# Kernel optimization log

Hardware: AMD Instinct MI355X
Metric: run time of the kernel (lower is better)

## Reference

```python
import jax, jax.numpy as jnp
import numpy as np

S = 2        # number of scales (init default)
ALPHA = 1.0  # loss weight (init default)


def _local_pod_ss(D, n_scales):
    """Sum of squares of (P_n - P_o) over all scales/windows.

    D = h_n - h_o, shape [B, C, W, H]. Because POD is linear in x,
    POD(h_n window) - POD(h_o window) == POD(D window), and the final
    torch.norm(P_n - P_o, 2) is the Frobenius norm over the full concat,
    so we accumulate squared window-POD values of D and sqrt at the end.
    Window sums are computed once via prefix sums (integral along one axis)
    instead of the original O(W^2 H^2) re-summation loop.
    """
    B, C, W, H = D.shape
    ss = jnp.zeros((), D.dtype)
    d = 1
    for s in range(n_scales):
        w, h = W // d, H // d
        if w == 0 or h == 0:
            break
        nI, nJ = W - w, H - h  # number of window start positions (torch range(0, W-w))
        if nI > 0 and nJ > 0:
            # 'left' term: sum over rows (dim=2) of each window, divided by w
            cs2 = jnp.pad(jnp.cumsum(D, axis=2), ((0, 0), (0, 0), (1, 0), (0, 0)))
            row = cs2[:, :, w:w + nI, :] - cs2[:, :, :nI, :]              # [B,C,nI,H]
            jidx = jnp.arange(nJ)[:, None] + jnp.arange(h)[None, :]       # [nJ,h]
            left = row[:, :, :, jidx] / w                                 # [B,C,nI,nJ,h]
            ss = ss + jnp.sum(left * left)
            # 'right' term: sum over cols (dim=3) of each window, divided by h
            cs3 = jnp.pad(jnp.cumsum(D, axis=3), ((0, 0), (0, 0), (0, 0), (1, 0)))
            col = cs3[:, :, :, h:h + nJ] - cs3[:, :, :, :nJ]              # [B,C,W,nJ]
            iidx = jnp.arange(nI)[:, None] + jnp.arange(w)[None, :]       # [nI,w]
            right = col[:, :, iidx, :] / h                                # [B,C,nI,w,nJ]
            ss = ss + jnp.sum(right * right)
        d *= 2
    return ss


def setup_inputs() -> dict:
    key = jax.random.key(0)
    k1, k2 = jax.random.split(key)
    new_f = jax.random.normal(k1, (16, 512, 32, 32), dtype=jnp.float32)
    old_f = jax.random.normal(k2, (16, 512, 32, 32), dtype=jnp.float32)
    return {"new_f": new_f, "old_f": old_f}


def reference(new_f, old_f):
    # forward loops over dict keys; here new_f/old_f model a single-key dict,
    # so loss = 1e-6 + local_pod(h_n, h_o) and divisor is len(new_f)+1 == 2.
    D = new_f - old_f
    loss = jnp.asarray(1e-6, new_f.dtype) + jnp.sqrt(_local_pod_ss(D, S))
    return ALPHA * loss / 2.0
```

## Files before the change

### kernel.cpp

```cpp
#include <hip/hip_runtime.h>
#include <math.h>


#define TILES_PER_BLOCK 8
#define TILE_STRIDE (32 * 33)

__global__ __launch_bounds__(256) void pod_partial(const float* __restrict__ nf,
                                                   const float* __restrict__ of,
                                                   float* __restrict__ partial) {
    __shared__ float ds[TILES_PER_BLOCK * TILE_STRIDE];
    const int tid = threadIdx.x;
    const size_t base = (size_t)blockIdx.x * (TILES_PER_BLOCK * 1024);

    const float4* nf4 = reinterpret_cast<const float4*>(nf + base);
    const float4* of4 = reinterpret_cast<const float4*>(of + base);
#pragma unroll
    for (int it = 0; it < (TILES_PER_BLOCK * 1024) / (256 * 4); ++it) {
        int e4 = it * 256 + tid;
        float4 a = nf4[e4];
        float4 b = of4[e4];
        int e = e4 * 4;
        int tile = e >> 10;
        int r = (e >> 5) & 31;
        int c = e & 31;
        float* dst = &ds[tile * TILE_STRIDE + r * 33 + c];
        dst[0] = a.x - b.x;
        dst[1] = a.y - b.y;
        dst[2] = a.z - b.z;
        dst[3] = a.w - b.w;
    }
    __syncthreads();

    float acc = 0.0f;

    {
        int tile = tid >> 5, col = tid & 31;
        const float* colp = &ds[tile * TILE_STRIDE + col];
        float v[32];
#pragma unroll
        for (int r = 0; r < 32; ++r) v[r] = colp[r * 33];
        float W = 0.0f;
#pragma unroll
        for (int r = 0; r < 16; ++r) W += v[r];
        float s2 = W * W;
#pragma unroll
        for (int i = 1; i < 16; ++i) { W += v[i + 15] - v[i - 1]; s2 += W * W; }
        float wl = (col < 16) ? (float)(col + 1) : (float)(31 - col);
        acc += wl * s2;
    }

    {
        int tile = tid >> 5, row = tid & 31;
        const float* rowp = &ds[tile * TILE_STRIDE + row * 33];
        float v[32];
#pragma unroll
        for (int c = 0; c < 32; ++c) v[c] = rowp[c];
        float W = 0.0f;
#pragma unroll
        for (int c = 0; c < 16; ++c) W += v[c];
        float s2 = W * W;
#pragma unroll
        for (int j = 1; j < 16; ++j) { W += v[j + 15] - v[j - 1]; s2 += W * W; }
        float wr = (row < 16) ? (float)(row + 1) : (float)(31 - row);
        acc += wr * s2;
    }

    acc *= (1.0f / 256.0f);

#pragma unroll
    for (int off = 32; off > 0; off >>= 1) acc += __shfl_down(acc, off, 64);
    __shared__ float wsum[4];
    if ((tid & 63) == 0) wsum[tid >> 6] = acc;
    __syncthreads();
    if (tid == 0) partial[blockIdx.x] = (wsum[0] + wsum[1]) + (wsum[2] + wsum[3]);
}

__global__ __launch_bounds__(256) void pod_final(const float* __restrict__ partial, int n,
                                                 float* __restrict__ out) {
    __shared__ float sh[256];
    int tid = threadIdx.x;
    float a = 0.0f;
    for (int i = tid; i < n; i += 256) a += partial[i];
    sh[tid] = a;
    __syncthreads();
    for (int s = 128; s > 0; s >>= 1) {
        if (tid < s) sh[tid] += sh[tid + s];
        __syncthreads();
    }
    if (tid == 0) out[0] = 0.5f * (1e-6f + sqrtf(sh[0]));
}

extern "C" void kernel_launch(void* const* d_in, const int* in_sizes, int n_in,
                              void* d_out, int out_size, void* d_ws, size_t ws_size,
                              hipStream_t stream) {
    const float* nf = (const float*)d_in[0];
    const float* of = (const float*)d_in[1];
    float* out = (float*)d_out;
    float* partial = (float*)d_ws;

    const int ntiles = 16 * 512;
    const int nblocks = ntiles / TILES_PER_BLOCK;

    hipLaunchKernelGGL(pod_partial, dim3(nblocks), dim3(256), 0, stream, nf, of, partial);
    hipLaunchKernelGGL(pod_final, dim3(1), dim3(256), 0, stream, partial, nblocks, out);
}
```

Baseline: 18.55 us.

## Fuse final reduction via last-block atomic counter and double-buffer tile chunks

Replaces the two-kernel partial and final reduction with one kernel in which the last block to finish, found through an atomic counter, sums the per-block partials. Each block now handles its 8 tiles as two chunks in separate shared-memory buffers, with the second chunk's global loads issued before the first chunk's compute so they overlap. Column and row work is now split across threads (half do columns, half rows) rather than each thread doing both. This adds a hipMemsetAsync on every call and a threadfence/atomic on every block. Block count is now derived from in_sizes, and the counter sits at the start of the workspace.

```diff
diff --git a/kernel.cpp b/kernel.cpp
--- a/kernel.cpp
+++ b/kernel.cpp
@@ -2,69 +2,88 @@
 #include <math.h>
 
 
-#define TILES_PER_BLOCK 8
-#define TILE_STRIDE (32 * 33)
+#define TILE_PAD 33
+#define TILE_STRIDE (32 * TILE_PAD)
+#define CHUNK_TILES 4
+#define TPB_TILES 8
+#define BLOCK_FLOATS (TPB_TILES * 1024)
 
-__global__ __launch_bounds__(256) void pod_partial(const float* __restrict__ nf,
-                                                   const float* __restrict__ of,
-                                                   float* __restrict__ partial) {
-    __shared__ float ds[TILES_PER_BLOCK * TILE_STRIDE];
+__device__ __forceinline__ float chunk_term(const float* __restrict__ buf, int tid) {
+    const int item = tid & 127;
+    const int tile = item >> 5;
+    const int lane = item & 31;
+    float v[32];
+    if (tid < 128) {
+        const float* p = &buf[tile * TILE_STRIDE + lane];
+#pragma unroll
+        for (int k = 0; k < 32; ++k) v[k] = p[k * TILE_PAD];
+    } else {
+        const float* p = &buf[tile * TILE_STRIDE + lane * TILE_PAD];
+#pragma unroll
+        for (int k = 0; k < 32; ++k) v[k] = p[k];
+    }
+    float W = 0.0f;
+#pragma unroll
+    for (int k = 0; k < 16; ++k) W += v[k];
+    float s2 = W * W;
+#pragma unroll
+    for (int i = 1; i < 16; ++i) { W += v[i + 15] - v[i - 1]; s2 += W * W; }
+    float wgt = (lane < 16) ? (float)(lane + 1) : (float)(31 - lane);
+    return wgt * s2;
+}
+
+__global__ __launch_bounds__(256) void pod_fused(const float* __restrict__ nf,
+                                                 const float* __restrict__ of,
+                                                 unsigned* __restrict__ counter,
+                                                 float* __restrict__ partial,
+                                                 float* __restrict__ out) {
+    __shared__ float ds[2][CHUNK_TILES * TILE_STRIDE];
     const int tid = threadIdx.x;
-    const size_t base = (size_t)blockIdx.x * (TILES_PER_BLOCK * 1024);
-
+    const size_t base = (size_t)blockIdx.x * BLOCK_FLOATS;
     const float4* nf4 = reinterpret_cast<const float4*>(nf + base);
     const float4* of4 = reinterpret_cast<const float4*>(of + base);
+
+    float4 a0[4], b0[4];
 #pragma unroll
-    for (int it = 0; it < (TILES_PER_BLOCK * 1024) / (256 * 4); ++it) {
+    for (int it = 0; it < 4; ++it) {
         int e4 = it * 256 + tid;
-        float4 a = nf4[e4];
-        float4 b = of4[e4];
-        int e = e4 * 4;
-        int tile = e >> 10;
-        int r = (e >> 5) & 31;
-        int c = e & 31;
-        float* dst = &ds[tile * TILE_STRIDE + r * 33 + c];
-        dst[0] = a.x - b.x;
-        dst[1] = a.y - b.y;
-        dst[2] = a.z - b.z;
-        dst[3] = a.w - b.w;
+        a0[it] = nf4[e4];
+        b0[it] = of4[e4];
+    }
+#pragma unroll
+    for (int it = 0; it < 4; ++it) {
+        int e = (it * 256 + tid) * 4;
+        int tile = e >> 10, r = (e >> 5) & 31, c = e & 31;
+        float* dst = &ds[0][tile * TILE_STRIDE + r * TILE_PAD + c];
+        dst[0] = a0[it].x - b0[it].x;
+        dst[1] = a0[it].y - b0[it].y;
+        dst[2] = a0[it].z - b0[it].z;
+        dst[3] = a0[it].w - b0[it].w;
+    }
+    float4 a1[4], b1[4];
+#pragma unroll
+    for (int it = 0; it < 4; ++it) {
+        int e4 = 1024 + it * 256 + tid;
+        a1[it] = nf4[e4];
+        b1[it] = of4[e4];
     }
     __syncthreads();
 
-    float acc = 0.0f;
+    float acc = chunk_term(&ds[0][0], tid);
 
-    {
-        int tile = tid >> 5, col = tid & 31;
-        const float* colp = &ds[tile * TILE_STRIDE + col];
-        float v[32];
 #pragma unroll
-        for (int r = 0; r < 32; ++r) v[r] = colp[r * 33];
-        float W = 0.0f;
-#pragma unroll
-        for (int r = 0; r < 16; ++r) W += v[r];
-        float s2 = W * W;
-#pragma unroll
-        for (int i = 1; i < 16; ++i) { W += v[i + 15] - v[i - 1]; s2 += W * W; }
-        float wl = (col < 16) ? (float)(col + 1) : (float)(31 - col);
-        acc += wl * s2;
+    for (int it = 0; it < 4; ++it) {
+        int e = (it * 256 + tid) * 4;
+        int tile = e >> 10, r = (e >> 5) & 31, c = e & 31;
+        float* dst = &ds[1][tile * TILE_STRIDE + r * TILE_PAD + c];
+        dst[0] = a1[it].x - b1[it].x;
+        dst[1] = a1[it].y - b1[it].y;
+        dst[2] = a1[it].z - b1[it].z;
+        dst[3] = a1[it].w - b1[it].w;
     }
+    __syncthreads();
 
-    {
-        int tile = tid >> 5, row = tid & 31;
-        const float* rowp = &ds[tile * TILE_STRIDE + row * 33];
-        float v[32];
-#pragma unroll
-        for (int c = 0; c < 32; ++c) v[c] = rowp[c];
-        float W = 0.0f;
-#pragma unroll
-        for (int c = 0; c < 16; ++c) W += v[c];
-        float s2 = W * W;
-#pragma unroll
-        for (int j = 1; j < 16; ++j) { W += v[j + 15] - v[j - 1]; s2 += W * W; }
-        float wr = (row < 16) ? (float)(row + 1) : (float)(31 - row);
-        acc += wr * s2;
-    }
-
+    acc += chunk_term(&ds[1][0], tid);
     acc *= (1.0f / 256.0f);
 
 #pragma unroll
@@ -72,22 +91,31 @@
     __shared__ float wsum[4];
     if ((tid & 63) == 0) wsum[tid >> 6] = acc;
     __syncthreads();
-    if (tid == 0) partial[blockIdx.x] = (wsum[0] + wsum[1]) + (wsum[2] + wsum[3]);
-}
 
-__global__ __launch_bounds__(256) void pod_final(const float* __restrict__ partial, int n,
-                                                 float* __restrict__ out) {
-    __shared__ float sh[256];
-    int tid = threadIdx.x;
-    float a = 0.0f;
-    for (int i = tid; i < n; i += 256) a += partial[i];
-    sh[tid] = a;
+    __shared__ unsigned last;
+    if (tid == 0) {
+        float total = (wsum[0] + wsum[1]) + (wsum[2] + wsum[3]);
+        partial[blockIdx.x] = total;
+        __threadfence();
+        unsigned old = atomicAdd(counter, 1u);
+        last = (old == gridDim.x - 1) ? 1u : 0u;
+    }
     __syncthreads();
-    for (int s = 128; s > 0; s >>= 1) {
-        if (tid < s) sh[tid] += sh[tid + s];
+
+    if (last) {
+        __threadfence();
+        float s = 0.0f;
+        for (unsigned i = tid; i < gridDim.x; i += 256)
+            s += partial[i];
+        __shared__ float sh[256];
+        sh[tid] = s;
         __syncthreads();
+        for (int st = 128; st > 0; st >>= 1) {
+            if (tid < st) sh[tid] += sh[tid + st];
+            __syncthreads();
+        }
+        if (tid == 0) out[0] = 0.5f * (1e-6f + sqrtf(sh[0]));
     }
-    if (tid == 0) out[0] = 0.5f * (1e-6f + sqrtf(sh[0]));
 }
 
 extern "C" void kernel_launch(void* const* d_in, const int* in_sizes, int n_in,
@@ -96,11 +124,13 @@
     const float* nf = (const float*)d_in[0];
     const float* of = (const float*)d_in[1];
     float* out = (float*)d_out;
-    float* partial = (float*)d_ws;
 
-    const int ntiles = 16 * 512;
-    const int nblocks = ntiles / TILES_PER_BLOCK;
+    unsigned* counter = (unsigned*)d_ws;
+    float* partial = (float*)d_ws + 64;
 
-    hipLaunchKernelGGL(pod_partial, dim3(nblocks), dim3(256), 0, stream, nf, of, partial);
-    hipLaunchKernelGGL(pod_final, dim3(1), dim3(256), 0, stream, partial, nblocks, out);
+    const int nblocks = in_sizes[0] / BLOCK_FLOATS;
+
+    hipMemsetAsync(counter, 0, sizeof(unsigned), stream);
+    hipLaunchKernelGGL(pod_fused, dim3(nblocks), dim3(256), 0, stream,
+                       nf, of, counter, partial, out);
 }
```

Result: slower. 53.04 us (+185.9%).

## Fuse final reduction into main kernel via fixed-point atomics and last-block finish

Applied to the files above, without the earlier changes.

Replaces the two-kernel partial-sum plus single-block final reduction with one kernel. Each block adds its partial into a 64-bit fixed-point atomic accumulator, and a completion counter lets the last block compute the sqrt output. All global loads are now issued up front into registers before the shared-memory stores, giving more memory-level parallelism. This removes a kernel launch and the serial tail reduction, but adds a memset, atomic contention, and quantization error from the fixed-point scaling; the ordering between the two atomics relies on an asm dependency trick rather than a fence.

```diff
diff --git a/kernel.cpp b/kernel.cpp
--- a/kernel.cpp
+++ b/kernel.cpp
@@ -2,32 +2,39 @@
 #include <math.h>
 
 
-#define TILES_PER_BLOCK 8
-#define TILE_STRIDE (32 * 33)
+#define TILE_PAD 33
+#define TILE_STRIDE (32 * TILE_PAD)
+#define NTILES 8
+#define BLOCK_FLOATS (NTILES * 1024)
+#define FP_SCALE 1048576.0f
 
-__global__ __launch_bounds__(256) void pod_partial(const float* __restrict__ nf,
-                                                   const float* __restrict__ of,
-                                                   float* __restrict__ partial) {
-    __shared__ float ds[TILES_PER_BLOCK * TILE_STRIDE];
+__global__ __launch_bounds__(256) void pod_fused(const float* __restrict__ nf,
+                                                 const float* __restrict__ of,
+                                                 unsigned long long* __restrict__ ssAcc,
+                                                 unsigned* __restrict__ counter,
+                                                 float* __restrict__ out,
+                                                 unsigned nblocks) {
+    __shared__ float ds[NTILES * TILE_STRIDE];
     const int tid = threadIdx.x;
-    const size_t base = (size_t)blockIdx.x * (TILES_PER_BLOCK * 1024);
-
+    const size_t base = (size_t)blockIdx.x * BLOCK_FLOATS;
     const float4* nf4 = reinterpret_cast<const float4*>(nf + base);
     const float4* of4 = reinterpret_cast<const float4*>(of + base);
+
+    float4 a[8], b[8];
 #pragma unroll
-    for (int it = 0; it < (TILES_PER_BLOCK * 1024) / (256 * 4); ++it) {
-        int e4 = it * 256 + tid;
-        float4 a = nf4[e4];
-        float4 b = of4[e4];
-        int e = e4 * 4;
-        int tile = e >> 10;
-        int r = (e >> 5) & 31;
-        int c = e & 31;
-        float* dst = &ds[tile * TILE_STRIDE + r * 33 + c];
-        dst[0] = a.x - b.x;
-        dst[1] = a.y - b.y;
-        dst[2] = a.z - b.z;
-        dst[3] = a.w - b.w;
+    for (int it = 0; it < 8; ++it) a[it] = nf4[it * 256 + tid];
+#pragma unroll
+    for (int it = 0; it < 8; ++it) b[it] = of4[it * 256 + tid];
+
+#pragma unroll
+    for (int it = 0; it < 8; ++it) {
+        int e = (it * 256 + tid) * 4;
+        int tile = e >> 10, r = (e >> 5) & 31, c = e & 31;
+        float* dst = &ds[tile * TILE_STRIDE + r * TILE_PAD + c];
+        dst[0] = a[it].x - b[it].x;
+        dst[1] = a[it].y - b[it].y;
+        dst[2] = a[it].z - b[it].z;
+        dst[3] = a[it].w - b[it].w;
     }
     __syncthreads();
 
@@ -35,10 +42,10 @@
 
     {
         int tile = tid >> 5, col = tid & 31;
-        const float* colp = &ds[tile * TILE_STRIDE + col];
+        const float* p = &ds[tile * TILE_STRIDE + col];
         float v[32];
 #pragma unroll
-        for (int r = 0; r < 32; ++r) v[r] = colp[r * 33];
+        for (int r = 0; r < 32; ++r) v[r] = p[r * TILE_PAD];
         float W = 0.0f;
 #pragma unroll
         for (int r = 0; r < 16; ++r) W += v[r];
@@ -51,10 +58,10 @@
 
     {
         int tile = tid >> 5, row = tid & 31;
-        const float* rowp = &ds[tile * TILE_STRIDE + row * 33];
+        const float* p = &ds[tile * TILE_STRIDE + row * TILE_PAD];
         float v[32];
 #pragma unroll
-        for (int c = 0; c < 32; ++c) v[c] = rowp[c];
+        for (int c = 0; c < 32; ++c) v[c] = p[c];
         float W = 0.0f;
 #pragma unroll
         for (int c = 0; c < 16; ++c) W += v[c];
@@ -72,22 +79,20 @@
     __shared__ float wsum[4];
     if ((tid & 63) == 0) wsum[tid >> 6] = acc;
     __syncthreads();
-    if (tid == 0) partial[blockIdx.x] = (wsum[0] + wsum[1]) + (wsum[2] + wsum[3]);
-}
 
-__global__ __launch_bounds__(256) void pod_final(const float* __restrict__ partial, int n,
-                                                 float* __restrict__ out) {
-    __shared__ float sh[256];
-    int tid = threadIdx.x;
-    float a = 0.0f;
-    for (int i = tid; i < n; i += 256) a += partial[i];
-    sh[tid] = a;
-    __syncthreads();
-    for (int s = 128; s > 0; s >>= 1) {
-        if (tid < s) sh[tid] += sh[tid + s];
-        __syncthreads();
+    if (tid == 0) {
+        float total = (wsum[0] + wsum[1]) + (wsum[2] + wsum[3]);
+        long long q = (long long)(total * FP_SCALE);
+        unsigned long long old = atomicAdd(ssAcc, (unsigned long long)q);
+        unsigned inc = 1u;
+        asm volatile("" : "+v"(inc) : "v"((unsigned)old));
+        unsigned done = atomicAdd(counter, inc);
+        if (done == nblocks - 1u) {
+            unsigned long long v = atomicAdd(ssAcc, 0ull);
+            float ss = (float)(long long)v * (1.0f / FP_SCALE);
+            out[0] = 0.5f * (1e-6f + sqrtf(ss));
+        }
     }
-    if (tid == 0) out[0] = 0.5f * (1e-6f + sqrtf(sh[0]));
 }
 
 extern "C" void kernel_launch(void* const* d_in, const int* in_sizes, int n_in,
@@ -96,11 +101,13 @@
     const float* nf = (const float*)d_in[0];
     const float* of = (const float*)d_in[1];
     float* out = (float*)d_out;
-    float* partial = (float*)d_ws;
 
-    const int ntiles = 16 * 512;
-    const int nblocks = ntiles / TILES_PER_BLOCK;
+    unsigned long long* ssAcc = (unsigned long long*)d_ws;
+    unsigned* counter = (unsigned*)((char*)d_ws + 8);
 
-    hipLaunchKernelGGL(pod_partial, dim3(nblocks), dim3(256), 0, stream, nf, of, partial);
-    hipLaunchKernelGGL(pod_final, dim3(1), dim3(256), 0, stream, partial, nblocks, out);
+    const unsigned nblocks = (unsigned)(in_sizes[0] / BLOCK_FLOATS);
+
+    hipMemsetAsync(d_ws, 0, 16, stream);
+    hipLaunchKernelGGL(pod_fused, dim3(nblocks), dim3(256), 0, stream,
+                       nf, of, ssAcc, counter, out, nblocks);
 }
```

Result: slower. 40.63 us (+119.0%).
